# Kernel optimization log

Measured on AMD Instinct MI355X. Metric: run time of the kernel, lower is better.

The kernel has to match this reference:

```python
import jax, jax.numpy as jnp
import numpy as np

B, TE, TD, D = 8, 2048, 2048, 256

def setup_inputs() -> dict:
    key = jax.random.key(0)
    k1, k2 = jax.random.split(key)
    encoder_outputs = jax.random.normal(k1, (B, TE, D), dtype=jnp.float32)
    decoder_outputs = jax.random.normal(k2, (B, TD, D), dtype=jnp.float32)
    return {"encoder_outputs": encoder_outputs, "decoder_outputs": decoder_outputs}

def reference(encoder_outputs, decoder_outputs):
    # luong_score[b,e,t] = sum_d enc[b,e,d] * dec[b,t,d]   (batch_dot with dec transposed)
    luong_score = jnp.einsum('bed,btd->bet', encoder_outputs, decoder_outputs)
    # softmax over encoder-time axis (axis=1)
    luong_score = jax.nn.softmax(luong_score, axis=1)
    # original does expand_dims + broadcast-multiply + sum over axis=1;
    # same math as a contraction over e: context[b,t,d] = sum_e score[b,e,t]*enc[b,e,d]
    encoder_vector = jnp.einsum('bet,bed->btd', luong_score, encoder_outputs)
    return jnp.concatenate([decoder_outputs, encoder_vector], axis=-1)
```

## Files before the change

kernel.cpp:

```cpp
#include <hip/hip_runtime.h>

typedef _Float16 f16;
typedef _Float16 f16x2 __attribute__((ext_vector_type(2)));
typedef _Float16 f16x4 __attribute__((ext_vector_type(4)));
typedef _Float16 f16x8 __attribute__((ext_vector_type(8)));
typedef float    f32x16 __attribute__((ext_vector_type(16)));

#define NB   8
#define TE   2048
#define TD   2048
#define DIM  256
#define NBTD (NB * TD)
#define LOG2E 1.44269504088896340736f

#define AS1(p) ((const __attribute__((address_space(1))) void*)(p))
#define AS3(p) ((__attribute__((address_space(3))) void*)(p))
#define MFMA32(a,b,c) __builtin_amdgcn_mfma_f32_32x32x16_f16((a),(b),(c),0,0,0)
#define SHUF8(x,y) __builtin_shufflevector((x),(y),0,1,2,3,4,5,6,7)

__device__ __forceinline__ unsigned lds_u32(void* p) {
    return (unsigned)(size_t)((__attribute__((address_space(3))) void*)p);
}
__device__ __forceinline__ f16x4 tr_rd0(unsigned a) {
    f16x4 r;
    asm volatile("ds_read_b64_tr_b16 %0, %1" : "=v"(r) : "v"(a));
    return r;
}
__device__ __forceinline__ f16x4 tr_rd1(unsigned a) {
    f16x4 r;
    asm volatile("ds_read_b64_tr_b16 %0, %1 offset:2048" : "=v"(r) : "v"(a));
    return r;
}

__global__ __launch_bounds__(256) void prep_kernel(const float* __restrict__ enc,
                                                   f16* __restrict__ ench) {
    size_t i = ((size_t)blockIdx.x * 256 + threadIdx.x) * 8;
    float4 v0 = *(const float4*)(enc + i);
    float4 v1 = *(const float4*)(enc + i + 4);
    f16x8 o;
    o[0]=(f16)v0.x; o[1]=(f16)v0.y; o[2]=(f16)v0.z; o[3]=(f16)v0.w;
    o[4]=(f16)v1.x; o[5]=(f16)v1.y; o[6]=(f16)v1.z; o[7]=(f16)v1.w;
    *(f16x8*)(ench + i) = o;
}

__global__ __launch_bounds__(256, 2) void attn_kernel(
        const float* __restrict__ dec32,
        const f16*  __restrict__ enc_h,
        f16*   __restrict__ ctxp,
        f16x2* __restrict__ ml,
        float* __restrict__ out) {
    __shared__ __align__(16) char lds[43008];
    const int tid  = threadIdx.x;
    const int lane = tid & 63;
    const int wv   = tid >> 6;
    const int t5   = lane & 31;
    const int hi   = lane >> 5;

    const int fid = blockIdx.x + 16 * (blockIdx.y + 8 * blockIdx.z);
    const int b    = fid & 7;
    const int rest = fid >> 3;
    const int xb   = rest & 15;
    const int z    = rest >> 4;
    const int t0   = xb * 128 + wv * 32;
    const int tile0 = z * 16;
    const int ITERS = 16;

    const char* encb = (const char*)(enc_h + (size_t)b * TE * DIM);

    const int c0  = wv * 64 + lane;
    const int e_l = ((c0 >> 7) << 2) | ((c0 >> 1) & 3);
    const int d_l = (((c0 >> 3) & 15) << 4) | ((c0 & 1) << 3);
    const int stage_goff = e_l * (DIM * 2) + d_l * 2;
    char* stage_dst = lds + wv * 1024;

    const int qk_base = ((lane & 31) >> 2) * 2048 + (lane & 3) * 32 + hi * 16;
    const unsigned tr_base = (unsigned)(hi * 4096 + ((lane >> 4) & 1) * 128 + (lane & 15) * 8);
    const unsigned lds_base = lds_u32(lds);
    char* pb = lds + 32768 + wv * 2560;

    f16x8 qf[16];
    {
        const float* qrow = dec32 + ((size_t)b * TD + t0 + t5) * DIM + hi * 8;
        #pragma unroll
        for (int ks = 0; ks < 16; ks++) {
            float4 u = *(const float4*)(qrow + ks * 16);
            float4 v = *(const float4*)(qrow + ks * 16 + 4);
            f16x8 o;
            o[0]=(f16)u.x; o[1]=(f16)u.y; o[2]=(f16)u.z; o[3]=(f16)u.w;
            o[4]=(f16)v.x; o[5]=(f16)v.y; o[6]=(f16)v.z; o[7]=(f16)v.w;
            qf[ks] = o;
        }
    }

    {
        const char* s = encb + (size_t)tile0 * 16384 + stage_goff;
        #pragma unroll
        for (int i = 0; i < 4; i++)
            __builtin_amdgcn_global_load_lds(AS1(s + i * 4096), AS3(stage_dst + i * 4096), 16, 0, 0);
    }

    float m_ = -INFINITY, l_ = 0.f;
    f32x16 ctx[8];
    #pragma unroll
    for (int dm = 0; dm < 8; dm++)
        #pragma unroll
        for (int r = 0; r < 16; r++) ctx[dm][r] = 0.f;

    __syncthreads();

    for (int it = 0; it < ITERS; ++it) {
        const int nat = (it & 1) << 14;
        if (it + 1 < ITERS) {
            const char* s = encb + (size_t)(tile0 + it + 1) * 16384 + stage_goff;
            char* dd = lds + (((it + 1) & 1) << 14) + wv * 1024;
            #pragma unroll
            for (int i = 0; i < 4; i++)
                __builtin_amdgcn_global_load_lds(AS1(s + i * 4096), AS3(dd + i * 4096), 16, 0, 0);
        }
        f32x16 st;
        #pragma unroll
        for (int r = 0; r < 16; r++) st[r] = 0.f;
        const char* natp = lds + nat + qk_base;
        #pragma unroll
        for (int ks = 0; ks < 16; ks++) {
            f16x8 af = *(const f16x8*)(natp + ks * 128);
            st = MFMA32(af, qf[ks], st);
        }
        float x0 = fmaxf(fmaxf(st[0], st[1]),  fmaxf(st[2], st[3]));
        float x1 = fmaxf(fmaxf(st[4], st[5]),  fmaxf(st[6], st[7]));
        float x2 = fmaxf(fmaxf(st[8], st[9]),  fmaxf(st[10], st[11]));
        float x3 = fmaxf(fmaxf(st[12], st[13]), fmaxf(st[14], st[15]));
        float mx = fmaxf(fmaxf(x0, x1), fmaxf(x2, x3));
        mx = fmaxf(mx, __shfl_xor(mx, 32, 64));
        float ms = (float)(f16)fmaxf(m_, mx);
        float al = __builtin_amdgcn_exp2f((m_ - ms) * LOG2E);
        bool bump = ms > m_;
        m_ = ms;
        float ssum = 0.f;
        #pragma unroll
        for (int g = 0; g < 4; g++) {
            f16x4 pv;
            #pragma unroll
            for (int r = 0; r < 4; r++) {
                float p = __builtin_amdgcn_exp2f((st[4 * g + r] - ms) * LOG2E);
                pv[r] = (f16)p;
                ssum += (float)pv[r];
            }
            *(f16x4*)(pb + t5 * 80 + g * 16 + hi * 8) = pv;
        }
        ssum += __shfl_xor(ssum, 32, 64);
        l_ = l_ * al + ssum;
        if (__any(bump)) {
            #pragma unroll
            for (int dm = 0; dm < 8; dm++)
                #pragma unroll
                for (int r = 0; r < 16; r++) ctx[dm][r] *= al;
        }
        const unsigned trb = lds_base + (unsigned)nat + tr_base;
        #pragma unroll
        for (int ks = 0; ks < 2; ks++) {
            f16x8 pf = *(const f16x8*)(pb + t5 * 80 + ks * 32 + hi * 16);
            const unsigned ab = trb + (unsigned)(ks * 8192);
            f16x4 a0 = tr_rd0(ab);        f16x4 a1 = tr_rd1(ab);
            f16x4 a2 = tr_rd0(ab + 256);  f16x4 a3 = tr_rd1(ab + 256);
            f16x4 a4 = tr_rd0(ab + 512);  f16x4 a5 = tr_rd1(ab + 512);
            f16x4 a6 = tr_rd0(ab + 768);  f16x4 a7 = tr_rd1(ab + 768);
            asm volatile("s_waitcnt lgkmcnt(0)" ::: "memory");
            __builtin_amdgcn_sched_barrier(0);
            ctx[0] = MFMA32(SHUF8(a0, a1), pf, ctx[0]);
            ctx[1] = MFMA32(SHUF8(a2, a3), pf, ctx[1]);
            ctx[2] = MFMA32(SHUF8(a4, a5), pf, ctx[2]);
            ctx[3] = MFMA32(SHUF8(a6, a7), pf, ctx[3]);
            f16x4 b0 = tr_rd0(ab + 1024); f16x4 b1 = tr_rd1(ab + 1024);
            f16x4 b2 = tr_rd0(ab + 1280); f16x4 b3 = tr_rd1(ab + 1280);
            f16x4 b4 = tr_rd0(ab + 1536); f16x4 b5 = tr_rd1(ab + 1536);
            f16x4 b6 = tr_rd0(ab + 1792); f16x4 b7 = tr_rd1(ab + 1792);
            asm volatile("s_waitcnt lgkmcnt(0)" ::: "memory");
            __builtin_amdgcn_sched_barrier(0);
            ctx[4] = MFMA32(SHUF8(b0, b1), pf, ctx[4]);
            ctx[5] = MFMA32(SHUF8(b2, b3), pf, ctx[5]);
            ctx[6] = MFMA32(SHUF8(b4, b5), pf, ctx[6]);
            ctx[7] = MFMA32(SHUF8(b6, b7), pf, ctx[7]);
        }
        __syncthreads();
    }

    const float inv = 1.0f / l_;
    if (z < 3) {
        f16* cb = ctxp + ((size_t)(z * NB + b) * TD + t0 + t5) * DIM;
        #pragma unroll
        for (int dm = 0; dm < 8; dm++)
            #pragma unroll
            for (int g = 0; g < 4; g++) {
                f16x4 cv;
                #pragma unroll
                for (int r = 0; r < 4; r++) cv[r] = (f16)(ctx[dm][4 * g + r] * inv);
                *(f16x4*)(cb + dm * 32 + g * 8 + hi * 4) = cv;
            }
    } else {
        float* ob = out + ((size_t)b * TD + t0 + t5) * 512 + 256;
        #pragma unroll
        for (int dm = 0; dm < 8; dm++)
            #pragma unroll
            for (int g = 0; g < 4; g++) {
                float4 cv;
                cv.x = ctx[dm][4 * g]     * inv;
                cv.y = ctx[dm][4 * g + 1] * inv;
                cv.z = ctx[dm][4 * g + 2] * inv;
                cv.w = ctx[dm][4 * g + 3] * inv;
                *(float4*)(ob + dm * 32 + g * 8 + hi * 4) = cv;
            }
    }
    if (hi == 0) {
        f16x2 v; v[0] = (f16)m_; v[1] = (f16)l_;
        ml[(size_t)z * NBTD + (size_t)b * TD + t0 + t5] = v;
    }
}

__global__ __launch_bounds__(256) void combine_kernel(const float* __restrict__ dec32,
        const f16* __restrict__ ctxp, const f16x2* __restrict__ ml,
        float* __restrict__ out) {
    int idx  = blockIdx.x * 256 + threadIdx.x;
    int trow = idx >> 5;
    int dg   = (idx & 31) * 8;
    float m0[4], l0[4], M = -INFINITY;
    #pragma unroll
    for (int s = 0; s < 4; s++) {
        f16x2 v = ml[(size_t)s * NBTD + trow];
        m0[s] = (float)v[0];
        l0[s] = (float)v[1];
        M = fmaxf(M, m0[s]);
    }
    float L = 0.f, w[4];
    #pragma unroll
    for (int s = 0; s < 4; s++) {
        w[s] = __builtin_amdgcn_exp2f((m0[s] - M) * LOG2E) * l0[s];
        L += w[s];
    }
    float invL = 1.0f / L;
    float acc[8] = {0.f,0.f,0.f,0.f,0.f,0.f,0.f,0.f};
    #pragma unroll
    for (int s = 0; s < 3; s++) {
        f16x8 v = *(const f16x8*)(ctxp + ((size_t)s * NBTD + trow) * DIM + dg);
        float ws = w[s] * invL;
        #pragma unroll
        for (int j = 0; j < 8; j++) acc[j] += ws * (float)v[j];
    }
    {
        const float* o3 = out + (size_t)trow * 512 + 256 + dg;
        float4 p0 = *(const float4*)(o3);
        float4 p1 = *(const float4*)(o3 + 4);
        float w3 = w[3] * invL;
        acc[0] += w3 * p0.x; acc[1] += w3 * p0.y; acc[2] += w3 * p0.z; acc[3] += w3 * p0.w;
        acc[4] += w3 * p1.x; acc[5] += w3 * p1.y; acc[6] += w3 * p1.z; acc[7] += w3 * p1.w;
    }
    float4 d0 = *(const float4*)(dec32 + (size_t)trow * DIM + dg);
    float4 d1 = *(const float4*)(dec32 + (size_t)trow * DIM + dg + 4);
    float* ob = out + (size_t)trow * 512;
    *(float4*)(ob + dg)     = d0;
    *(float4*)(ob + dg + 4) = d1;
    float4 c0, c1;
    c0.x=acc[0]; c0.y=acc[1]; c0.z=acc[2]; c0.w=acc[3];
    c1.x=acc[4]; c1.y=acc[5]; c1.z=acc[6]; c1.w=acc[7];
    *(float4*)(ob + 256 + dg)     = c0;
    *(float4*)(ob + 256 + dg + 4) = c1;
}

extern "C" void kernel_launch(void* const* d_in, const int* in_sizes, int n_in,
                              void* d_out, int out_size, void* d_ws, size_t ws_size,
                              hipStream_t stream) {
    (void)in_sizes; (void)n_in;
    const float* enc = (const float*)d_in[0];
    const float* dec = (const float*)d_in[1];
    float* out = (float*)d_out;

    const size_t MLB = (size_t)4 * NBTD * 4;
    const size_t HB  = (size_t)NB * TE * DIM * 2;
    const size_t CSL = (size_t)NBTD * DIM * 2;
    const size_t NEED = MLB + HB + 3 * CSL;

    if (ws_size < NEED) {
        hipMemsetAsync(d_out, 0, (size_t)out_size * sizeof(float), stream);
        return;
    }
    f16x2* ml   = (f16x2*)d_ws;
    f16*   ench = (f16*)((char*)d_ws + MLB);
    f16*   ctxp = (f16*)((char*)d_ws + MLB + HB);

    prep_kernel<<<2048, 256, 0, stream>>>(enc, ench);
    attn_kernel<<<dim3(16, 8, 4), 256, 0, stream>>>(dec, ench, ctxp, ml, out);
    combine_kernel<<<2048, 256, 0, stream>>>(dec, ctxp, ml, out);
}
```

Before: 145.6 us.

## Switch attention to 16x16 MFMA tiles with 3-way encoder split and higher occupancy

Replaces the 32x32x16 MFMA tiling with 16x16x32 MFMA, so each wave handles 16 decoder rows instead of 32. Each wave's accumulator shrinks and LDS per block drops, which lets the kernel target 3 blocks per CU. The encoder sequence is now split 3 ways instead of 4, giving a grid of 768 blocks. Partial results go to one f16 workspace slice plus both halves of the output buffer, which shrinks the workspace and the combine traffic. The costs are smaller MFMA tiles with less operand reuse per instruction, and uneven tile counts across the splits.

```diff
diff --git a/kernel.cpp b/kernel.cpp
--- a/kernel.cpp
+++ b/kernel.cpp
@@ -4,7 +4,7 @@
 typedef _Float16 f16x2 __attribute__((ext_vector_type(2)));
 typedef _Float16 f16x4 __attribute__((ext_vector_type(4)));
 typedef _Float16 f16x8 __attribute__((ext_vector_type(8)));
-typedef float    f32x16 __attribute__((ext_vector_type(16)));
+typedef float    f32x4 __attribute__((ext_vector_type(4)));
 
 #define NB   8
 #define TE   2048
@@ -15,7 +15,7 @@
 
 #define AS1(p) ((const __attribute__((address_space(1))) void*)(p))
 #define AS3(p) ((__attribute__((address_space(3))) void*)(p))
-#define MFMA32(a,b,c) __builtin_amdgcn_mfma_f32_32x32x16_f16((a),(b),(c),0,0,0)
+#define MFMA16(a,b,c) __builtin_amdgcn_mfma_f32_16x16x32_f16((a),(b),(c),0,0,0)
 #define SHUF8(x,y) __builtin_shufflevector((x),(y),0,1,2,3,4,5,6,7)
 
 __device__ __forceinline__ unsigned lds_u32(void* p) {
@@ -43,27 +43,26 @@
     *(f16x8*)(ench + i) = o;
 }
 
-__global__ __launch_bounds__(256, 2) void attn_kernel(
+__global__ __launch_bounds__(256, 3) void attn_kernel(
         const float* __restrict__ dec32,
         const f16*  __restrict__ enc_h,
         f16*   __restrict__ ctxp,
         f16x2* __restrict__ ml,
         float* __restrict__ out) {
-    __shared__ __align__(16) char lds[43008];
+    __shared__ __align__(16) char lds[37888];
     const int tid  = threadIdx.x;
     const int lane = tid & 63;
     const int wv   = tid >> 6;
-    const int t5   = lane & 31;
-    const int hi   = lane >> 5;
-
-    const int fid = blockIdx.x + 16 * (blockIdx.y + 8 * blockIdx.z);
-    const int b    = fid & 7;
-    const int rest = fid >> 3;
-    const int xb   = rest & 15;
-    const int z    = rest >> 4;
-    const int t0   = xb * 128 + wv * 32;
-    const int tile0 = z * 16;
-    const int ITERS = 16;
+    const int tcol = lane & 15;
+    const int q    = lane >> 4;
+
+    const int x  = blockIdx.x;
+    const int b  = x & 7;
+    const int xb = (x >> 3) | (blockIdx.y << 2);
+    const int z  = blockIdx.z;
+    const int t0 = xb * 64 + wv * 16;
+    const int tile0 = (64 * z) / 3;
+    const int iters = (64 * (z + 1)) / 3 - tile0;
 
     const char* encb = (const char*)(enc_h + (size_t)b * TE * DIM);
 
@@ -73,18 +72,19 @@
     const int stage_goff = e_l * (DIM * 2) + d_l * 2;
     char* stage_dst = lds + wv * 1024;
 
-    const int qk_base = ((lane & 31) >> 2) * 2048 + (lane & 3) * 32 + hi * 16;
-    const unsigned tr_base = (unsigned)(hi * 4096 + ((lane >> 4) & 1) * 128 + (lane & 15) * 8);
+    const int qk_b0 = (tcol >> 2) * 2048 + (q >> 1) * 128 + (tcol & 3) * 32 + (q & 1) * 16;
+    const int qk_b1 = qk_b0 + 8192;
+    const unsigned tr_base = (unsigned)(q * 4096 + tcol * 8);
     const unsigned lds_base = lds_u32(lds);
-    char* pb = lds + 32768 + wv * 2560;
-
-    f16x8 qf[16];
-    {
-        const float* qrow = dec32 + ((size_t)b * TD + t0 + t5) * DIM + hi * 8;
-        #pragma unroll
-        for (int ks = 0; ks < 16; ks++) {
-            float4 u = *(const float4*)(qrow + ks * 16);
-            float4 v = *(const float4*)(qrow + ks * 16 + 4);
+    char* pb = lds + 32768 + wv * 1280;
+
+    f16x8 qf[8];
+    {
+        const float* qrow = dec32 + ((size_t)b * TD + t0 + tcol) * DIM + q * 8;
+        #pragma unroll
+        for (int ks = 0; ks < 8; ks++) {
+            float4 u = *(const float4*)(qrow + ks * 32);
+            float4 v = *(const float4*)(qrow + ks * 32 + 4);
             f16x8 o;
             o[0]=(f16)u.x; o[1]=(f16)u.y; o[2]=(f16)u.z; o[3]=(f16)u.w;
             o[4]=(f16)v.x; o[5]=(f16)v.y; o[6]=(f16)v.z; o[7]=(f16)v.w;
@@ -99,121 +99,104 @@
             __builtin_amdgcn_global_load_lds(AS1(s + i * 4096), AS3(stage_dst + i * 4096), 16, 0, 0);
     }
 
+    const f32x4 zero4 = {0.f, 0.f, 0.f, 0.f};
     float m_ = -INFINITY, l_ = 0.f;
-    f32x16 ctx[8];
+    f32x4 ctx[16];
     #pragma unroll
-    for (int dm = 0; dm < 8; dm++)
-        #pragma unroll
-        for (int r = 0; r < 16; r++) ctx[dm][r] = 0.f;
+    for (int dm = 0; dm < 16; dm++) ctx[dm] = zero4;
 
     __syncthreads();
 
-    for (int it = 0; it < ITERS; ++it) {
+    for (int it = 0; it < iters; ++it) {
         const int nat = (it & 1) << 14;
-        if (it + 1 < ITERS) {
+        if (it + 1 < iters) {
             const char* s = encb + (size_t)(tile0 + it + 1) * 16384 + stage_goff;
             char* dd = lds + (((it + 1) & 1) << 14) + wv * 1024;
             #pragma unroll
             for (int i = 0; i < 4; i++)
                 __builtin_amdgcn_global_load_lds(AS1(s + i * 4096), AS3(dd + i * 4096), 16, 0, 0);
         }
-        f32x16 st;
-        #pragma unroll
-        for (int r = 0; r < 16; r++) st[r] = 0.f;
-        const char* natp = lds + nat + qk_base;
-        #pragma unroll
-        for (int ks = 0; ks < 16; ks++) {
-            f16x8 af = *(const f16x8*)(natp + ks * 128);
-            st = MFMA32(af, qf[ks], st);
-        }
-        float x0 = fmaxf(fmaxf(st[0], st[1]),  fmaxf(st[2], st[3]));
-        float x1 = fmaxf(fmaxf(st[4], st[5]),  fmaxf(st[6], st[7]));
-        float x2 = fmaxf(fmaxf(st[8], st[9]),  fmaxf(st[10], st[11]));
-        float x3 = fmaxf(fmaxf(st[12], st[13]), fmaxf(st[14], st[15]));
-        float mx = fmaxf(fmaxf(x0, x1), fmaxf(x2, x3));
+        f32x4 st0 = zero4, st1 = zero4;
+        const char* natp = lds + nat;
+        #pragma unroll
+        for (int ks = 0; ks < 8; ks++) {
+            f16x8 af0 = *(const f16x8*)(natp + qk_b0 + ks * 256);
+            f16x8 af1 = *(const f16x8*)(natp + qk_b1 + ks * 256);
+            st0 = MFMA16(af0, qf[ks], st0);
+            st1 = MFMA16(af1, qf[ks], st1);
+        }
+        float mx = fmaxf(fmaxf(fmaxf(st0[0], st0[1]), fmaxf(st0[2], st0[3])),
+                         fmaxf(fmaxf(st1[0], st1[1]), fmaxf(st1[2], st1[3])));
+        mx = fmaxf(mx, __shfl_xor(mx, 16, 64));
         mx = fmaxf(mx, __shfl_xor(mx, 32, 64));
         float ms = (float)(f16)fmaxf(m_, mx);
         float al = __builtin_amdgcn_exp2f((m_ - ms) * LOG2E);
         bool bump = ms > m_;
         m_ = ms;
+        f16x4 pv0, pv1;
         float ssum = 0.f;
         #pragma unroll
-        for (int g = 0; g < 4; g++) {
-            f16x4 pv;
-            #pragma unroll
-            for (int r = 0; r < 4; r++) {
-                float p = __builtin_amdgcn_exp2f((st[4 * g + r] - ms) * LOG2E);
-                pv[r] = (f16)p;
-                ssum += (float)pv[r];
-            }
-            *(f16x4*)(pb + t5 * 80 + g * 16 + hi * 8) = pv;
-        }
+        for (int r = 0; r < 4; r++) {
+            float p0 = __builtin_amdgcn_exp2f((st0[r] - ms) * LOG2E);
+            float p1 = __builtin_amdgcn_exp2f((st1[r] - ms) * LOG2E);
+            pv0[r] = (f16)p0; pv1[r] = (f16)p1;
+            ssum += (float)pv0[r] + (float)pv1[r];
+        }
+        *(f16x4*)(pb + tcol * 80 + q * 8)      = pv0;
+        *(f16x4*)(pb + tcol * 80 + 32 + q * 8) = pv1;
+        ssum += __shfl_xor(ssum, 16, 64);
         ssum += __shfl_xor(ssum, 32, 64);
         l_ = l_ * al + ssum;
         if (__any(bump)) {
             #pragma unroll
-            for (int dm = 0; dm < 8; dm++)
-                #pragma unroll
-                for (int r = 0; r < 16; r++) ctx[dm][r] *= al;
-        }
+            for (int dm = 0; dm < 16; dm++) {
+                ctx[dm][0] *= al; ctx[dm][1] *= al;
+                ctx[dm][2] *= al; ctx[dm][3] *= al;
+            }
+        }
+        f16x8 pf = *(const f16x8*)(pb + tcol * 80 + q * 16);
         const unsigned trb = lds_base + (unsigned)nat + tr_base;
         #pragma unroll
-        for (int ks = 0; ks < 2; ks++) {
-            f16x8 pf = *(const f16x8*)(pb + t5 * 80 + ks * 32 + hi * 16);
-            const unsigned ab = trb + (unsigned)(ks * 8192);
+        for (int bb = 0; bb < 4; bb++) {
+            const unsigned ab = trb + (unsigned)(bb * 512);
             f16x4 a0 = tr_rd0(ab);        f16x4 a1 = tr_rd1(ab);
-            f16x4 a2 = tr_rd0(ab + 256);  f16x4 a3 = tr_rd1(ab + 256);
-            f16x4 a4 = tr_rd0(ab + 512);  f16x4 a5 = tr_rd1(ab + 512);
-            f16x4 a6 = tr_rd0(ab + 768);  f16x4 a7 = tr_rd1(ab + 768);
+            f16x4 a2 = tr_rd0(ab + 128);  f16x4 a3 = tr_rd1(ab + 128);
+            f16x4 a4 = tr_rd0(ab + 256);  f16x4 a5 = tr_rd1(ab + 256);
+            f16x4 a6 = tr_rd0(ab + 384);  f16x4 a7 = tr_rd1(ab + 384);
             asm volatile("s_waitcnt lgkmcnt(0)" ::: "memory");
             __builtin_amdgcn_sched_barrier(0);
-            ctx[0] = MFMA32(SHUF8(a0, a1), pf, ctx[0]);
-            ctx[1] = MFMA32(SHUF8(a2, a3), pf, ctx[1]);
-            ctx[2] = MFMA32(SHUF8(a4, a5), pf, ctx[2]);
-            ctx[3] = MFMA32(SHUF8(a6, a7), pf, ctx[3]);
-            f16x4 b0 = tr_rd0(ab + 1024); f16x4 b1 = tr_rd1(ab + 1024);
-            f16x4 b2 = tr_rd0(ab + 1280); f16x4 b3 = tr_rd1(ab + 1280);
-            f16x4 b4 = tr_rd0(ab + 1536); f16x4 b5 = tr_rd1(ab + 1536);
-            f16x4 b6 = tr_rd0(ab + 1792); f16x4 b7 = tr_rd1(ab + 1792);
-            asm volatile("s_waitcnt lgkmcnt(0)" ::: "memory");
-            __builtin_amdgcn_sched_barrier(0);
-            ctx[4] = MFMA32(SHUF8(b0, b1), pf, ctx[4]);
-            ctx[5] = MFMA32(SHUF8(b2, b3), pf, ctx[5]);
-            ctx[6] = MFMA32(SHUF8(b4, b5), pf, ctx[6]);
-            ctx[7] = MFMA32(SHUF8(b6, b7), pf, ctx[7]);
+            ctx[bb * 4 + 0] = MFMA16(SHUF8(a0, a1), pf, ctx[bb * 4 + 0]);
+            ctx[bb * 4 + 1] = MFMA16(SHUF8(a2, a3), pf, ctx[bb * 4 + 1]);
+            ctx[bb * 4 + 2] = MFMA16(SHUF8(a4, a5), pf, ctx[bb * 4 + 2]);
+            ctx[bb * 4 + 3] = MFMA16(SHUF8(a6, a7), pf, ctx[bb * 4 + 3]);
         }
         __syncthreads();
     }
 
     const float inv = 1.0f / l_;
-    if (z < 3) {
-        f16* cb = ctxp + ((size_t)(z * NB + b) * TD + t0 + t5) * DIM;
-        #pragma unroll
-        for (int dm = 0; dm < 8; dm++)
+    const size_t row = (size_t)b * TD + t0 + tcol;
+    if (z == 0) {
+        f16* cb = ctxp + row * DIM;
+        #pragma unroll
+        for (int dm = 0; dm < 16; dm++) {
+            f16x4 cv;
             #pragma unroll
-            for (int g = 0; g < 4; g++) {
-                f16x4 cv;
-                #pragma unroll
-                for (int r = 0; r < 4; r++) cv[r] = (f16)(ctx[dm][4 * g + r] * inv);
-                *(f16x4*)(cb + dm * 32 + g * 8 + hi * 4) = cv;
-            }
+            for (int r = 0; r < 4; r++) cv[r] = (f16)(ctx[dm][r] * inv);
+            *(f16x4*)(cb + dm * 16 + q * 4) = cv;
+        }
     } else {
-        float* ob = out + ((size_t)b * TD + t0 + t5) * 512 + 256;
-        #pragma unroll
-        for (int dm = 0; dm < 8; dm++)
-            #pragma unroll
-            for (int g = 0; g < 4; g++) {
-                float4 cv;
-                cv.x = ctx[dm][4 * g]     * inv;
-                cv.y = ctx[dm][4 * g + 1] * inv;
-                cv.z = ctx[dm][4 * g + 2] * inv;
-                cv.w = ctx[dm][4 * g + 3] * inv;
-                *(float4*)(ob + dm * 32 + g * 8 + hi * 4) = cv;
-            }
-    }
-    if (hi == 0) {
+        float* ob = out + row * 512 + (z == 2 ? 256 : 0);
+        #pragma unroll
+        for (int dm = 0; dm < 16; dm++) {
+            float4 cv;
+            cv.x = ctx[dm][0] * inv; cv.y = ctx[dm][1] * inv;
+            cv.z = ctx[dm][2] * inv; cv.w = ctx[dm][3] * inv;
+            *(float4*)(ob + dm * 16 + q * 4) = cv;
+        }
+    }
+    if (q == 0) {
         f16x2 v; v[0] = (f16)m_; v[1] = (f16)l_;
-        ml[(size_t)z * NBTD + (size_t)b * TD + t0 + t5] = v;
+        ml[(size_t)z * NBTD + row] = v;
     }
 }
 
@@ -223,36 +206,43 @@
     int idx  = blockIdx.x * 256 + threadIdx.x;
     int trow = idx >> 5;
     int dg   = (idx & 31) * 8;
-    float m0[4], l0[4], M = -INFINITY;
+    float m0[3], l0[3], M = -INFINITY;
     #pragma unroll
-    for (int s = 0; s < 4; s++) {
+    for (int s = 0; s < 3; s++) {
         f16x2 v = ml[(size_t)s * NBTD + trow];
         m0[s] = (float)v[0];
         l0[s] = (float)v[1];
         M = fmaxf(M, m0[s]);
     }
-    float L = 0.f, w[4];
+    float L = 0.f, w[3];
     #pragma unroll
-    for (int s = 0; s < 4; s++) {
+    for (int s = 0; s < 3; s++) {
         w[s] = __builtin_amdgcn_exp2f((m0[s] - M) * LOG2E) * l0[s];
         L += w[s];
     }
     float invL = 1.0f / L;
-    float acc[8] = {0.f,0.f,0.f,0.f,0.f,0.f,0.f,0.f};
-    #pragma unroll
-    for (int s = 0; s < 3; s++) {
-        f16x8 v = *(const f16x8*)(ctxp + ((size_t)s * NBTD + trow) * DIM + dg);
-        float ws = w[s] * invL;
-        #pragma unroll
-        for (int j = 0; j < 8; j++) acc[j] += ws * (float)v[j];
-    }
-    {
-        const float* o3 = out + (size_t)trow * 512 + 256 + dg;
-        float4 p0 = *(const float4*)(o3);
-        float4 p1 = *(const float4*)(o3 + 4);
-        float w3 = w[3] * invL;
-        acc[0] += w3 * p0.x; acc[1] += w3 * p0.y; acc[2] += w3 * p0.z; acc[3] += w3 * p0.w;
-        acc[4] += w3 * p1.x; acc[5] += w3 * p1.y; acc[6] += w3 * p1.z; acc[7] += w3 * p1.w;
+    float acc[8];
+    {
+        f16x8 v = *(const f16x8*)(ctxp + (size_t)trow * DIM + dg);
+        float w0 = w[0] * invL;
+        #pragma unroll
+        for (int j = 0; j < 8; j++) acc[j] = w0 * (float)v[j];
+    }
+    {
+        const float* o1 = out + (size_t)trow * 512 + dg;
+        float4 p0 = *(const float4*)(o1);
+        float4 p1 = *(const float4*)(o1 + 4);
+        float w1 = w[1] * invL;
+        acc[0] += w1 * p0.x; acc[1] += w1 * p0.y; acc[2] += w1 * p0.z; acc[3] += w1 * p0.w;
+        acc[4] += w1 * p1.x; acc[5] += w1 * p1.y; acc[6] += w1 * p1.z; acc[7] += w1 * p1.w;
+    }
+    {
+        const float* o2 = out + (size_t)trow * 512 + 256 + dg;
+        float4 p0 = *(const float4*)(o2);
+        float4 p1 = *(const float4*)(o2 + 4);
+        float w2 = w[2] * invL;
+        acc[0] += w2 * p0.x; acc[1] += w2 * p0.y; acc[2] += w2 * p0.z; acc[3] += w2 * p0.w;
+        acc[4] += w2 * p1.x; acc[5] += w2 * p1.y; acc[6] += w2 * p1.z; acc[7] += w2 * p1.w;
     }
     float4 d0 = *(const float4*)(dec32 + (size_t)trow * DIM + dg);
     float4 d1 = *(const float4*)(dec32 + (size_t)trow * DIM + dg + 4);
@@ -274,10 +264,10 @@
     const float* dec = (const float*)d_in[1];
     float* out = (float*)d_out;
 
-    const size_t MLB = (size_t)4 * NBTD * 4;
+    const size_t MLB = (size_t)3 * NBTD * 4;
     const size_t HB  = (size_t)NB * TE * DIM * 2;
     const size_t CSL = (size_t)NBTD * DIM * 2;
-    const size_t NEED = MLB + HB + 3 * CSL;
+    const size_t NEED = MLB + HB + CSL;
 
     if (ws_size < NEED) {
         hipMemsetAsync(d_out, 0, (size_t)out_size * sizeof(float), stream);
@@ -288,6 +278,6 @@
     f16*   ctxp = (f16*)((char*)d_ws + MLB + HB);
 
     prep_kernel<<<2048, 256, 0, stream>>>(enc, ench);
-    attn_kernel<<<dim3(16, 8, 4), 256, 0, stream>>>(dec, ench, ctxp, ml, out);
+    attn_kernel<<<dim3(32, 8, 3), 256, 0, stream>>>(dec, ench, ctxp, ml, out);
     combine_kernel<<<2048, 256, 0, stream>>>(dec, ctxp, ml, out);
 }
```

Result: slower. 148.8 us (+2.1%).

## Fuse split-K combine into attention kernel via last-block atomic counter

Applied to the files above, without the earlier changes.

Removes the separate combine kernel. Each attention block bumps a per-(batch, row-tile) atomic counter, and the last of the four split blocks merges the partial contexts. Two partials now go straight to fp32 in the output buffer (the decoder half and the context half), so only two fp16 partial slices are kept in the workspace. This cuts one kernel launch and some workspace traffic. In exchange it adds a counter memset, threadfences, and a serial merge tail that runs on only 128 blocks.

```diff
diff --git a/kernel.cpp b/kernel.cpp
--- a/kernel.cpp
+++ b/kernel.cpp
@@ -48,8 +48,10 @@
         const f16*  __restrict__ enc_h,
         f16*   __restrict__ ctxp,
         f16x2* __restrict__ ml,
-        float* __restrict__ out) {
+        float* __restrict__ out,
+        unsigned* __restrict__ cnt) {
     __shared__ __align__(16) char lds[43008];
+    __shared__ int do_merge;
     const int tid  = threadIdx.x;
     const int lane = tid & 63;
     const int wv   = tid >> 6;
@@ -186,8 +188,9 @@
     }
 
     const float inv = 1.0f / l_;
-    if (z < 3) {
-        f16* cb = ctxp + ((size_t)(z * NB + b) * TD + t0 + t5) * DIM;
+    const size_t row = (size_t)b * TD + t0 + t5;
+    if (z < 2) {
+        f16* cb = ctxp + ((size_t)z * NBTD + row) * DIM;
         #pragma unroll
         for (int dm = 0; dm < 8; dm++)
             #pragma unroll
@@ -198,7 +201,7 @@
                 *(f16x4*)(cb + dm * 32 + g * 8 + hi * 4) = cv;
             }
     } else {
-        float* ob = out + ((size_t)b * TD + t0 + t5) * 512 + 256;
+        float* ob = out + row * 512 + (z == 3 ? 256 : 0);
         #pragma unroll
         for (int dm = 0; dm < 8; dm++)
             #pragma unroll
@@ -213,57 +216,76 @@
     }
     if (hi == 0) {
         f16x2 v; v[0] = (f16)m_; v[1] = (f16)l_;
-        ml[(size_t)z * NBTD + (size_t)b * TD + t0 + t5] = v;
-    }
-}
-
-__global__ __launch_bounds__(256) void combine_kernel(const float* __restrict__ dec32,
-        const f16* __restrict__ ctxp, const f16x2* __restrict__ ml,
-        float* __restrict__ out) {
-    int idx  = blockIdx.x * 256 + threadIdx.x;
-    int trow = idx >> 5;
-    int dg   = (idx & 31) * 8;
-    float m0[4], l0[4], M = -INFINITY;
-    #pragma unroll
-    for (int s = 0; s < 4; s++) {
-        f16x2 v = ml[(size_t)s * NBTD + trow];
-        m0[s] = (float)v[0];
-        l0[s] = (float)v[1];
-        M = fmaxf(M, m0[s]);
-    }
-    float L = 0.f, w[4];
-    #pragma unroll
-    for (int s = 0; s < 4; s++) {
-        w[s] = __builtin_amdgcn_exp2f((m0[s] - M) * LOG2E) * l0[s];
-        L += w[s];
-    }
-    float invL = 1.0f / L;
-    float acc[8] = {0.f,0.f,0.f,0.f,0.f,0.f,0.f,0.f};
-    #pragma unroll
-    for (int s = 0; s < 3; s++) {
-        f16x8 v = *(const f16x8*)(ctxp + ((size_t)s * NBTD + trow) * DIM + dg);
-        float ws = w[s] * invL;
-        #pragma unroll
-        for (int j = 0; j < 8; j++) acc[j] += ws * (float)v[j];
-    }
-    {
-        const float* o3 = out + (size_t)trow * 512 + 256 + dg;
-        float4 p0 = *(const float4*)(o3);
-        float4 p1 = *(const float4*)(o3 + 4);
-        float w3 = w[3] * invL;
-        acc[0] += w3 * p0.x; acc[1] += w3 * p0.y; acc[2] += w3 * p0.z; acc[3] += w3 * p0.w;
-        acc[4] += w3 * p1.x; acc[5] += w3 * p1.y; acc[6] += w3 * p1.z; acc[7] += w3 * p1.w;
-    }
-    float4 d0 = *(const float4*)(dec32 + (size_t)trow * DIM + dg);
-    float4 d1 = *(const float4*)(dec32 + (size_t)trow * DIM + dg + 4);
-    float* ob = out + (size_t)trow * 512;
-    *(float4*)(ob + dg)     = d0;
-    *(float4*)(ob + dg + 4) = d1;
-    float4 c0, c1;
-    c0.x=acc[0]; c0.y=acc[1]; c0.z=acc[2]; c0.w=acc[3];
-    c1.x=acc[4]; c1.y=acc[5]; c1.z=acc[6]; c1.w=acc[7];
-    *(float4*)(ob + 256 + dg)     = c0;
-    *(float4*)(ob + 256 + dg + 4) = c1;
+        ml[(size_t)z * NBTD + row] = v;
+    }
+
+    __threadfence();
+    __syncthreads();
+    if (tid == 0) {
+        unsigned old = atomicAdd(&cnt[b * 16 + xb], 1u);
+        do_merge = (old == 3u);
+    }
+    __syncthreads();
+    if (do_merge) {
+        __threadfence();
+        const size_t rbase = (size_t)b * TD + xb * 128;
+        for (int i = 0; i < 16; i++) {
+            int idx2 = i * 256 + tid;
+            int tl = idx2 >> 5;
+            int dg = (idx2 & 31) * 8;
+            size_t trow = rbase + tl;
+            float m0[4], l0[4], M = -INFINITY;
+            #pragma unroll
+            for (int s = 0; s < 4; s++) {
+                f16x2 v = ml[(size_t)s * NBTD + trow];
+                m0[s] = (float)v[0];
+                l0[s] = (float)v[1];
+                M = fmaxf(M, m0[s]);
+            }
+            float L = 0.f, w[4];
+            #pragma unroll
+            for (int s = 0; s < 4; s++) {
+                w[s] = __builtin_amdgcn_exp2f((m0[s] - M) * LOG2E) * l0[s];
+                L += w[s];
+            }
+            float invL = 1.0f / L;
+            float acc[8];
+            {
+                f16x8 v = *(const f16x8*)(ctxp + (size_t)trow * DIM + dg);
+                float w0 = w[0] * invL;
+                #pragma unroll
+                for (int j = 0; j < 8; j++) acc[j] = w0 * (float)v[j];
+                f16x8 u = *(const f16x8*)(ctxp + ((size_t)NBTD + trow) * DIM + dg);
+                float w1 = w[1] * invL;
+                #pragma unroll
+                for (int j = 0; j < 8; j++) acc[j] += w1 * (float)u[j];
+            }
+            float* ob = out + (size_t)trow * 512;
+            {
+                float4 p0 = *(const float4*)(ob + dg);
+                float4 p1 = *(const float4*)(ob + dg + 4);
+                float w2 = w[2] * invL;
+                acc[0] += w2 * p0.x; acc[1] += w2 * p0.y; acc[2] += w2 * p0.z; acc[3] += w2 * p0.w;
+                acc[4] += w2 * p1.x; acc[5] += w2 * p1.y; acc[6] += w2 * p1.z; acc[7] += w2 * p1.w;
+            }
+            {
+                float4 p0 = *(const float4*)(ob + 256 + dg);
+                float4 p1 = *(const float4*)(ob + 256 + dg + 4);
+                float w3 = w[3] * invL;
+                acc[0] += w3 * p0.x; acc[1] += w3 * p0.y; acc[2] += w3 * p0.z; acc[3] += w3 * p0.w;
+                acc[4] += w3 * p1.x; acc[5] += w3 * p1.y; acc[6] += w3 * p1.z; acc[7] += w3 * p1.w;
+            }
+            float4 d0 = *(const float4*)(dec32 + (size_t)trow * DIM + dg);
+            float4 d1 = *(const float4*)(dec32 + (size_t)trow * DIM + dg + 4);
+            *(float4*)(ob + dg)     = d0;
+            *(float4*)(ob + dg + 4) = d1;
+            float4 c0, c1;
+            c0.x=acc[0]; c0.y=acc[1]; c0.z=acc[2]; c0.w=acc[3];
+            c1.x=acc[4]; c1.y=acc[5]; c1.z=acc[6]; c1.w=acc[7];
+            *(float4*)(ob + 256 + dg)     = c0;
+            *(float4*)(ob + 256 + dg + 4) = c1;
+        }
+    }
 }
 
 extern "C" void kernel_launch(void* const* d_in, const int* in_sizes, int n_in,
@@ -274,20 +296,22 @@
     const float* dec = (const float*)d_in[1];
     float* out = (float*)d_out;
 
-    const size_t MLB = (size_t)4 * NBTD * 4;
-    const size_t HB  = (size_t)NB * TE * DIM * 2;
-    const size_t CSL = (size_t)NBTD * DIM * 2;
-    const size_t NEED = MLB + HB + 3 * CSL;
+    const size_t MLB  = (size_t)4 * NBTD * 4;
+    const size_t HB   = (size_t)NB * TE * DIM * 2;
+    const size_t C2   = (size_t)2 * NBTD * DIM * 2;
+    const size_t CNTB = 512;
+    const size_t NEED = MLB + HB + C2 + CNTB;
 
     if (ws_size < NEED) {
         hipMemsetAsync(d_out, 0, (size_t)out_size * sizeof(float), stream);
         return;
     }
-    f16x2* ml   = (f16x2*)d_ws;
-    f16*   ench = (f16*)((char*)d_ws + MLB);
-    f16*   ctxp = (f16*)((char*)d_ws + MLB + HB);
-
+    f16x2*    ml   = (f16x2*)d_ws;
+    f16*      ench = (f16*)((char*)d_ws + MLB);
+    f16*      ctxp = (f16*)((char*)d_ws + MLB + HB);
+    unsigned* cnt  = (unsigned*)((char*)d_ws + MLB + HB + C2);
+
+    hipMemsetAsync(cnt, 0, CNTB, stream);
     prep_kernel<<<2048, 256, 0, stream>>>(enc, ench);
-    attn_kernel<<<dim3(16, 8, 4), 256, 0, stream>>>(dec, ench, ctxp, ml, out);
-    combine_kernel<<<2048, 256, 0, stream>>>(dec, ctxp, ml, out);
-}
+    attn_kernel<<<dim3(16, 8, 4), 256, 0, stream>>>(dec, ench, ctxp, ml, out, cnt);
+}
```

Result: slower. 230.0 us (+57.9%).
